# Kernel optimization log

Hardware: AMD Instinct MI355X
Metric: run time of the kernel (lower is better)

## Reference

```python
import jax, jax.numpy as jnp
import numpy as np

N, E, D, L, H = 10000, 160000, 128, 3, 8
DH = D // H
EPS = 1e-5


def ln(x, g, b):
    m = x.mean(-1, keepdims=True)
    v = ((x - m) ** 2).mean(-1, keepdims=True)
    return (x - m) * jax.lax.rsqrt(v + EPS) * g + b


def setup_inputs() -> dict:
    key = jax.random.key(0)
    ks = iter(jax.random.split(key, 16))
    rn = lambda s, sc=0.05: jax.random.normal(next(ks), s, dtype=jnp.float32) * sc
    return {
        'lane_feats': jax.random.normal(next(ks), (N, 10), dtype=jnp.float32),
        'edge_attrs': jax.random.normal(next(ks), (E, 9), dtype=jnp.float32),
        'edge_index': jax.random.randint(next(ks), (2, E), 0, N),
        'node_W': rn((10, D)), 'node_b': jnp.zeros((D,)), 'node_g': jnp.ones((D,)), 'node_bt': jnp.zeros((D,)),
        'rpe_W': rn((9, D)), 'rpe_b': jnp.zeros((D,)), 'rpe_g': jnp.ones((D,)), 'rpe_bt': jnp.zeros((D,)),
        'mem_W': rn((L, 3 * D, D)), 'mem_b': jnp.zeros((L, D)), 'mem_g': jnp.ones((L, D)), 'mem_bt': jnp.zeros((L, D)),
        'Wq': rn((L, D, D)), 'Wk': rn((L, D, D)), 'Wv': rn((L, D, D)), 'Wo': rn((L, D, D)),
        'eu_W': rn((L, D, D)), 'eu_b': jnp.zeros((L, D)), 'eu_g': jnp.ones((L, D)), 'eu_bt': jnp.zeros((L, D)),
        'en_g': jnp.ones((L, D)), 'en_bt': jnp.zeros((L, D)),
        'ffn_W1': rn((L, D, 2 * D)), 'ffn_b1': jnp.zeros((L, 2 * D)),
        'ffn_W2': rn((L, 2 * D, D)), 'ffn_b2': jnp.zeros((L, D)),
        'n1_g': jnp.ones((L, D)), 'n1_bt': jnp.zeros((L, D)),
        'n2_g': jnp.ones((L, D)), 'n2_bt': jnp.zeros((L, D)),
    }


def reference(lane_feats, edge_attrs, edge_index,
              node_W, node_b, node_g, node_bt,
              rpe_W, rpe_b, rpe_g, rpe_bt,
              mem_W, mem_b, mem_g, mem_bt,
              Wq, Wk, Wv, Wo,
              eu_W, eu_b, eu_g, eu_bt,
              en_g, en_bt,
              ffn_W1, ffn_b1, ffn_W2, ffn_b2,
              n1_g, n1_bt, n2_g, n2_bt):
    src, dst = edge_index[0], edge_index[1]
    # input projections (dropout is identity in eval)
    x = jax.nn.relu(ln(lane_feats @ node_W + node_b, node_g, node_bt))  # [N, D]
    e = jax.nn.relu(ln(edge_attrs @ rpe_W + rpe_b, rpe_g, rpe_bt))      # [E, D]
    for l in range(L):
        x_i, x_j = x[dst], x[src]  # receiver / sender features [E, D]
        mem = jax.nn.relu(ln(jnp.concatenate([x_i, x_j, e], axis=-1) @ mem_W[l] + mem_b[l],
                             mem_g[l], mem_bt[l]))
        delta = jax.nn.relu(ln(mem @ eu_W[l] + eu_b[l], eu_g[l], eu_bt[l]))
        e = ln(e + delta, en_g[l], en_bt[l])
        q = (x_i @ Wq[l]).reshape(E, H, DH)
        k = (mem @ Wk[l]).reshape(E, H, DH)
        v = (mem @ Wv[l]).reshape(E, H, DH)
        logits = (q * k).sum(-1) / np.float32(np.sqrt(DH))  # [E, H]
        # segment softmax over destination nodes (pyg_softmax)
        mx = jax.ops.segment_max(logits, dst, num_segments=N)
        ex = jnp.exp(logits - mx[dst])
        sm = jax.ops.segment_sum(ex, dst, num_segments=N)
        attn = ex / (sm[dst] + 1e-16)
        out_e = (attn[..., None] * v).reshape(E, D) @ Wo[l]
        agg = jax.ops.segment_sum(out_e, dst, num_segments=N)  # scatter-add aggregation
        x = ln(x + agg, n1_g[l], n1_bt[l])
        h = jax.nn.relu(x @ ffn_W1[l] + ffn_b1[l]) @ ffn_W2[l] + ffn_b2[l]
        x = ln(x + h, n2_g[l], n2_bt[l])
    return x
```

## Files before the change

### kernel.cpp

```cpp
#include <hip/hip_runtime.h>
#include <cstdint>

#define NN 10000
#define NE 160000
#define DD 128
#define NL 3

typedef __attribute__((ext_vector_type(8))) __bf16 bf16x8;
typedef __attribute__((ext_vector_type(4))) float f32x4;

__device__ __forceinline__ ushort f2bf(float f) {
  unsigned u = __float_as_uint(f);
  return (ushort)((u + 0x7fffu + ((u >> 16) & 1u)) >> 16);
}
__device__ __forceinline__ float bf2f(ushort s) {
  return __uint_as_float(((unsigned)s) << 16);
}
__device__ __forceinline__ float wsum32(float v) {
  v += __shfl_xor(v, 1); v += __shfl_xor(v, 2); v += __shfl_xor(v, 4);
  v += __shfl_xor(v, 8); v += __shfl_xor(v, 16);
  return v;
}
__device__ __forceinline__ float wsum64(float v) {
  v = wsum32(v); v += __shfl_xor(v, 32); return v;
}
__device__ __forceinline__ void red16_2(float& a, float& b) {
#pragma unroll
  for (int m = 1; m < 16; m <<= 1) { a += __shfl_xor(a, m); b += __shfl_xor(b, m); }
}
__device__ __forceinline__ uint4 ldg16(const ushort* p) { return *(const uint4*)p; }

#define PH(id, MAXID, AT, ASTR, KK, AS) {                                       \
    if ((id) < (MAXID)) {                                                       \
      ushort* _db = Bb[((id) + 1) & 1];                                         \
      if ((id) & 1) { *(uint4*)(_db + tid * 8) = sa0;                           \
                      *(uint4*)(_db + 2048 + tid * 8) = sa1; }                  \
      else          { *(uint4*)(_db + tid * 8) = sb0;                           \
                      *(uint4*)(_db + 2048 + tid * 8) = sb1; }                  \
    }                                                                           \
    if ((id) + 2 <= (MAXID)) {                                                  \
      if ((id) & 1) { sb0 = ldg16(csrc((id) + 2, tid));                         \
                      sb1 = ldg16(csrc((id) + 2, 256 + tid)); }                 \
      else          { sa0 = ldg16(csrc((id) + 2, tid));                         \
                      sa1 = ldg16(csrc((id) + 2, 256 + tid)); }                 \
    }                                                                           \
    { bf16x8 _a = *(const bf16x8*)((AT) + (r0 + c) * (ASTR) + (KK) * 32 + g * 8); \
      const ushort* _bp = Bb[(id) & 1] + lane * 8;                              \
      __builtin_amdgcn_s_setprio(1);                                            \
      _Pragma("unroll") for (int _t = 0; _t < 8; ++_t)                          \
        AS[_t] = __builtin_amdgcn_mfma_f32_16x16x32_bf16(                       \
            _a, *(const bf16x8*)(_bp + _t * 512), AS[_t], 0, 0, 0);             \
      __builtin_amdgcn_s_setprio(0); }                                          \
    __syncthreads(); }

__global__ __launch_bounds__(256) void k_hist(const int* __restrict__ dst,
                                              int* __restrict__ deg) {
  int e = blockIdx.x * 256 + threadIdx.x;
  if (e < NE) atomicAdd(&deg[dst[e]], 1);
}

__global__ __launch_bounds__(256) void k_scan(const int* __restrict__ deg,
                                              int* __restrict__ rowptr,
                                              int* __restrict__ cursor) {
  __shared__ int part[256];
  const int t = threadIdx.x;
  const int CH = 40;
  int base = t * CH;
  int s = 0;
  for (int i = 0; i < CH; ++i) {
    int idx = base + i;
    s += (idx < NN) ? deg[idx] : 0;
  }
  part[t] = s;
  __syncthreads();
  for (int off = 1; off < 256; off <<= 1) {
    int v = (t >= off) ? part[t - off] : 0;
    __syncthreads();
    part[t] += v;
    __syncthreads();
  }
  int run = (t == 0) ? 0 : part[t - 1];
  for (int i = 0; i < CH; ++i) {
    int idx = base + i;
    if (idx < NN) {
      rowptr[idx] = run;
      cursor[idx] = run;
      run += deg[idx];
    }
  }
  if (t == 255) rowptr[NN] = part[255];
}

__global__ __launch_bounds__(256) void k_scatter(const int* __restrict__ dst,
                                                 int* __restrict__ cursor,
                                                 int* __restrict__ eids) {
  int e = blockIdx.x * 256 + threadIdx.x;
  if (e < NE) {
    int pos = atomicAdd(&cursor[dst[e]], 1);
    eids[pos] = e;
  }
}

__global__ __launch_bounds__(256) void k_permidx(const int* __restrict__ ei,
                                                 const int* __restrict__ perm,
                                                 int* __restrict__ srcP,
                                                 int* __restrict__ dstP) {
  int i = blockIdx.x * 256 + threadIdx.x;
  if (i < NE) {
    int e = perm[i];
    srcP[i] = ei[e];
    dstP[i] = ei[NE + e];
  }
}

__global__ __launch_bounds__(256) void k_transp(const float* __restrict__ in,
                                                ushort* __restrict__ out,
                                                int K, int N) {
  __shared__ float T[32][33];
  int k0 = blockIdx.x * 32, n0 = blockIdx.y * 32;
  in += (size_t)blockIdx.z * K * N;
  out += (size_t)blockIdx.z * K * N;
  int tx = threadIdx.x & 31, ty = threadIdx.x >> 5;
#pragma unroll
  for (int r = 0; r < 32; r += 8)
    if (k0 + ty + r < K && n0 + tx < N)
      T[ty + r][tx] = in[(size_t)(k0 + ty + r) * N + n0 + tx];
  __syncthreads();
#pragma unroll
  for (int r = 0; r < 32; r += 8)
    if (n0 + ty + r < N && k0 + tx < K)
      out[(size_t)(n0 + ty + r) * K + k0 + tx] = f2bf(T[tx][ty + r]);
}

__global__ __launch_bounds__(256) void k_transp5(
    const float* __restrict__ Wa, const float* __restrict__ Wb,
    const float* __restrict__ Wc, const float* __restrict__ Wd,
    const float* __restrict__ We, ushort* __restrict__ Oa,
    ushort* __restrict__ Ob, ushort* __restrict__ Oc, ushort* __restrict__ Od,
    ushort* __restrict__ Oe) {
  __shared__ float T[32][33];
  int l = blockIdx.z / 5, wsel = blockIdx.z % 5;
  const float* in =
      (wsel == 0 ? Wa : wsel == 1 ? Wb : wsel == 2 ? Wc : wsel == 3 ? Wd : We) +
      (size_t)l * 128 * 128;
  ushort* out =
      (wsel == 0 ? Oa : wsel == 1 ? Ob : wsel == 2 ? Oc : wsel == 3 ? Od : Oe) +
      (size_t)l * 128 * 128;
  int k0 = blockIdx.x * 32, n0 = blockIdx.y * 32;
  int tx = threadIdx.x & 31, ty = threadIdx.x >> 5;
#pragma unroll
  for (int r = 0; r < 32; r += 8)
    T[ty + r][tx] = in[(size_t)(k0 + ty + r) * 128 + n0 + tx];
  __syncthreads();
#pragma unroll
  for (int r = 0; r < 32; r += 8)
    out[(size_t)(n0 + ty + r) * 128 + k0 + tx] = f2bf(T[tx][ty + r]);
}

template <int K>
__global__ __launch_bounds__(256) void k_inproj(
    const float* __restrict__ inp, const int* __restrict__ perm,
    const float* __restrict__ W, const float* __restrict__ b,
    const float* __restrict__ g, const float* __restrict__ bt,
    float* __restrict__ outF, ushort* __restrict__ outB, int rows) {
  int row = blockIdx.x * 4 + (threadIdx.x >> 6);
  if (row >= rows) return;
  int srow = perm ? perm[row] : row;
  int lane = threadIdx.x & 63;
  float a0 = b[lane], a1 = b[lane + 64];
#pragma unroll
  for (int k = 0; k < K; ++k) {
    float xv = inp[(size_t)srow * K + k];
    a0 = fmaf(xv, W[k * DD + lane], a0);
    a1 = fmaf(xv, W[k * DD + lane + 64], a1);
  }
  float m = wsum64(a0 + a1) * (1.0f / DD);
  float q = wsum64(a0 * a0 + a1 * a1) * (1.0f / DD);
  float rstd = rsqrtf(q - m * m + 1e-5f);
  float o0 = fmaxf((a0 - m) * rstd * g[lane] + bt[lane], 0.0f);
  float o1 = fmaxf((a1 - m) * rstd * g[lane + 64] + bt[lane + 64], 0.0f);
  size_t base = (size_t)row * DD;
  if (outF) { outF[base + lane] = o0; outF[base + lane + 64] = o1; }
  outB[base + lane] = f2bf(o0);
  outB[base + lane + 64] = f2bf(o1);
}

__global__ __launch_bounds__(256) void k_nodepre(
    const ushort* __restrict__ xb, const ushort* __restrict__ memWT,
    const ushort* __restrict__ WqT, const float* __restrict__ memB,
    float* __restrict__ Pa, float* __restrict__ Pb, ushort* __restrict__ qbo) {
  __shared__ __align__(16) ushort Xt[64 * 136];
  __shared__ __align__(16) ushort Bb[4096];
  const int tid = threadIdx.x;
  const int n0 = blockIdx.x * 64;
  const int z = blockIdx.y;
  const ushort* B0 = (z == 0) ? memWT : ((z == 1) ? memWT + 128 : WqT);
  const int bstr = (z < 2) ? 384 : 128;
  uint4 w[2], wn[2];
#pragma unroll
  for (int i = 0; i < 2; ++i) {
    int u = tid + i * 256;
    w[i] = ldg16(B0 + (size_t)(u >> 2) * bstr + (u & 3) * 8);
  }
#pragma unroll
  for (int it = 0; it < 4; ++it) {
    int ch = it * 256 + tid, row = ch >> 4, j = ch & 15;
    int gr = n0 + row; if (gr > NN - 1) gr = NN - 1;
    *(uint4*)(Xt + row * 136 + j * 8) = *(const uint4*)(xb + (size_t)gr * DD + j * 8);
  }
  const int lane = tid & 63, wv = tid >> 6;
  const int c = lane & 15, g = lane >> 4, r0 = wv * 16;
  f32x4 acc[8];
#pragma unroll
  for (int t = 0; t < 8; ++t) acc[t] = (f32x4){0.f, 0.f, 0.f, 0.f};
#pragma unroll
  for (int kk = 0; kk < 4; ++kk) {
    __syncthreads();
#pragma unroll
    for (int i = 0; i < 2; ++i) *(uint4*)(Bb + (tid + i * 256) * 8) = w[i];
    if (kk < 3) {
#pragma unroll
      for (int i = 0; i < 2; ++i) {
        int u = tid + i * 256;
        wn[i] = ldg16(B0 + (size_t)(u >> 2) * bstr + (kk + 1) * 32 + (u & 3) * 8);
      }
    }
    __syncthreads();
    bf16x8 a = *(const bf16x8*)(Xt + (r0 + c) * 136 + kk * 32 + g * 8);
#pragma unroll
    for (int t = 0; t < 8; ++t)
      acc[t] = __builtin_amdgcn_mfma_f32_16x16x32_bf16(
          a, *(const bf16x8*)(Bb + (t * 16 + c) * 32 + g * 8), acc[t], 0, 0, 0);
#pragma unroll
    for (int i = 0; i < 2; ++i) w[i] = wn[i];
  }
  if (z == 0) {
#pragma unroll
    for (int t = 0; t < 8; ++t) {
      float bv = memB[t * 16 + c];
#pragma unroll
      for (int rr = 0; rr < 4; ++rr) {
        int row = n0 + r0 + g * 4 + rr;
        if (row < NN) Pa[(size_t)row * DD + t * 16 + c] = acc[t][rr] + bv;
      }
    }
  } else if (z == 1) {
#pragma unroll
    for (int t = 0; t < 8; ++t)
#pragma unroll
      for (int rr = 0; rr < 4; ++rr) {
        int row = n0 + r0 + g * 4 + rr;
        if (row < NN) Pb[(size_t)row * DD + t * 16 + c] = acc[t][rr];
      }
  } else {
#pragma unroll
    for (int t = 0; t < 8; ++t)
#pragma unroll
      for (int rr = 0; rr < 4; ++rr) {
        int row = n0 + r0 + g * 4 + rr;
        if (row < NN) qbo[(size_t)row * DD + t * 16 + c] = f2bf(acc[t][rr]);
      }
  }
}

__global__ __launch_bounds__(256, 3) void k_edge(
    ushort* __restrict__ ebg, ushort* __restrict__ vbg,
    const float* __restrict__ Pa, const float* __restrict__ Pb,
    const ushort* __restrict__ qb, const int* __restrict__ srcP,
    const int* __restrict__ dstP, const ushort* __restrict__ memWT,
    const float* __restrict__ memG, const float* __restrict__ memBt,
    const ushort* __restrict__ euWT, const float* __restrict__ euB,
    const float* __restrict__ euG, const float* __restrict__ euBt,
    const float* __restrict__ enG, const float* __restrict__ enBt,
    const ushort* __restrict__ WkT, const ushort* __restrict__ WvT,
    float* __restrict__ lg) {
  __shared__ __align__(16) ushort Et[64 * 136];
  __shared__ __align__(16) ushort Mt[64 * 136];
  __shared__ __align__(16) ushort Bb[2][4096];
  const int tid = threadIdx.x;
  const int e0 = blockIdx.x * 64;
  const int lane = tid & 63, wv = tid >> 6;
  const int c = lane & 15, g = lane >> 4, r0 = wv * 16;

  auto csrc = [&](int j, int u) -> const ushort* {
    const ushort* base; int stride, off, kk = j & 3;
    if (j < 4)       { base = memWT; stride = 384; off = 256 + kk * 32; }
    else if (j < 8)  { base = euWT;  stride = 128; off = kk * 32; }
    else if (j < 12) { base = WkT;   stride = 128; off = kk * 32; }
    else             { base = WvT;   stride = 128; off = kk * 32; }
    return base + ((u >> 6) * 16 + (u & 15)) * stride + off + ((u >> 4) & 3) * 8;
  };

  int dv[4], sv[4];
#pragma unroll
  for (int rr = 0; rr < 4; ++rr) {
    int row = e0 + r0 + g * 4 + rr;
    dv[rr] = dstP[row]; sv[rr] = srcP[row];
  }
  uint4 sa0 = ldg16(csrc(0, tid)), sa1 = ldg16(csrc(0, 256 + tid));
  uint4 sb0 = ldg16(csrc(1, tid)), sb1 = ldg16(csrc(1, 256 + tid));
#pragma unroll
  for (int it = 0; it < 4; ++it) {
    int ch = it * 256 + tid, row = ch >> 4, j = ch & 15;
    *(uint4*)(Et + row * 136 + j * 8) =
        *(const uint4*)(ebg + (size_t)(e0 + row) * DD + j * 8);
  }
  *(uint4*)(Bb[0] + tid * 8) = sa0;
  *(uint4*)(Bb[0] + 2048 + tid * 8) = sa1;
  __syncthreads();

  f32x4 acc[8];

#pragma unroll
  for (int t = 0; t < 8; ++t) acc[t] = (f32x4){0.f, 0.f, 0.f, 0.f};
  PH(0, 15, Et, 136, 0, acc)
  PH(1, 15, Et, 136, 1, acc)
  PH(2, 15, Et, 136, 2, acc)
  PH(3, 15, Et, 136, 3, acc)

  {
    float ps[8][4];
#pragma unroll
    for (int t = 0; t < 8; ++t)
#pragma unroll
      for (int rr = 0; rr < 4; ++rr)
        ps[t][rr] = Pa[(size_t)dv[rr] * DD + t * 16 + c] +
                    Pb[(size_t)sv[rr] * DD + t * 16 + c];
    float s1[4] = {0, 0, 0, 0}, s2[4] = {0, 0, 0, 0};
#pragma unroll
    for (int t = 0; t < 8; ++t)
#pragma unroll
      for (int rr = 0; rr < 4; ++rr) {
        float s = acc[t][rr] + ps[t][rr];
        acc[t][rr] = s; s1[rr] += s; s2[rr] += s * s;
      }
    float mean[4], rstd[4];
#pragma unroll
    for (int rr = 0; rr < 4; ++rr) {
      red16_2(s1[rr], s2[rr]);
      mean[rr] = s1[rr] * (1.f / DD);
      rstd[rr] = rsqrtf(s2[rr] * (1.f / DD) - mean[rr] * mean[rr] + 1e-5f);
    }
#pragma unroll
    for (int t = 0; t < 8; ++t) {
      float gv = memG[t * 16 + c], tv = memBt[t * 16 + c];
#pragma unroll
      for (int rr = 0; rr < 4; ++rr) {
        float o = fmaxf((acc[t][rr] - mean[rr]) * rstd[rr] * gv + tv, 0.f);
        Mt[(r0 + g * 4 + rr) * 136 + t * 16 + c] = f2bf(o);
      }
    }
  }
  __syncthreads();

#pragma unroll
  for (int t = 0; t < 8; ++t) acc[t] = (f32x4){0.f, 0.f, 0.f, 0.f};
  PH(4, 15, Mt, 136, 0, acc)
  PH(5, 15, Mt, 136, 1, acc)
  PH(6, 15, Mt, 136, 2, acc)
  PH(7, 15, Mt, 136, 3, acc)

  {
    float s1[4] = {0, 0, 0, 0}, s2[4] = {0, 0, 0, 0};
#pragma unroll
    for (int t = 0; t < 8; ++t) {
      float bv = euB[t * 16 + c];
#pragma unroll
      for (int rr = 0; rr < 4; ++rr) {
        float v2 = acc[t][rr] + bv;
        acc[t][rr] = v2; s1[rr] += v2; s2[rr] += v2 * v2;
      }
    }
    float mean[4], rstd[4];
#pragma unroll
    for (int rr = 0; rr < 4; ++rr) {
      red16_2(s1[rr], s2[rr]);
      mean[rr] = s1[rr] * (1.f / DD);
      rstd[rr] = rsqrtf(s2[rr] * (1.f / DD) - mean[rr] * mean[rr] + 1e-5f);
    }
    float t1[4] = {0, 0, 0, 0}, t2[4] = {0, 0, 0, 0};
#pragma unroll
    for (int t = 0; t < 8; ++t) {
      float gv = euG[t * 16 + c], tv = euBt[t * 16 + c];
#pragma unroll
      for (int rr = 0; rr < 4; ++rr) {
        float d = fmaxf((acc[t][rr] - mean[rr]) * rstd[rr] * gv + tv, 0.f);
        float eo = bf2f(Et[(r0 + g * 4 + rr) * 136 + t * 16 + c]);
        float pv = eo + d;
        acc[t][rr] = pv; t1[rr] += pv; t2[rr] += pv * pv;
      }
    }
    float mean3[4], rstd3[4];
#pragma unroll
    for (int rr = 0; rr < 4; ++rr) {
      red16_2(t1[rr], t2[rr]);
      mean3[rr] = t1[rr] * (1.f / DD);
      rstd3[rr] = rsqrtf(t2[rr] * (1.f / DD) - mean3[rr] * mean3[rr] + 1e-5f);
    }
#pragma unroll
    for (int t = 0; t < 8; ++t) {
      float gv = enG[t * 16 + c], tv = enBt[t * 16 + c];
#pragma unroll
      for (int rr = 0; rr < 4; ++rr) {
        float en = (acc[t][rr] - mean3[rr]) * rstd3[rr] * gv + tv;
        Et[(r0 + g * 4 + rr) * 136 + t * 16 + c] = f2bf(en);
      }
    }
  }
  __syncthreads();
#pragma unroll
  for (int it = 0; it < 4; ++it) {
    int ch = it * 256 + tid, row = ch >> 4, j = ch & 15;
    *(uint4*)(ebg + (size_t)(e0 + row) * DD + j * 8) =
        *(const uint4*)(Et + row * 136 + j * 8);
  }

  float qvf[8][4];
#pragma unroll
  for (int t = 0; t < 8; ++t)
#pragma unroll
    for (int rr = 0; rr < 4; ++rr)
      qvf[t][rr] = bf2f(qb[(size_t)dv[rr] * DD + t * 16 + c]);

#pragma unroll
  for (int t = 0; t < 8; ++t) acc[t] = (f32x4){0.f, 0.f, 0.f, 0.f};
  PH(8, 15, Mt, 136, 0, acc)
  PH(9, 15, Mt, 136, 1, acc)
  PH(10, 15, Mt, 136, 2, acc)
  PH(11, 15, Mt, 136, 3, acc)
#pragma unroll
  for (int t = 0; t < 8; ++t) {
    float p[4];
#pragma unroll
    for (int rr = 0; rr < 4; ++rr) p[rr] = acc[t][rr] * qvf[t][rr];
#pragma unroll
    for (int m = 1; m < 16; m <<= 1)
#pragma unroll
      for (int rr = 0; rr < 4; ++rr) p[rr] += __shfl_xor(p[rr], m);
    if (c == t) {
#pragma unroll
      for (int rr = 0; rr < 4; ++rr)
        lg[(size_t)(e0 + r0 + g * 4 + rr) * 8 + t] = p[rr] * 0.25f;
    }
  }

#pragma unroll
  for (int t = 0; t < 8; ++t) acc[t] = (f32x4){0.f, 0.f, 0.f, 0.f};
  PH(12, 15, Mt, 136, 0, acc)
  PH(13, 15, Mt, 136, 1, acc)
  PH(14, 15, Mt, 136, 2, acc)
  PH(15, 15, Mt, 136, 3, acc)
#pragma unroll
  for (int t = 0; t < 8; ++t)
#pragma unroll
    for (int rr = 0; rr < 4; ++rr)
      Et[(r0 + g * 4 + rr) * 136 + t * 16 + c] = f2bf(acc[t][rr]);
  __syncthreads();
#pragma unroll
  for (int it = 0; it < 4; ++it) {
    int ch = it * 256 + tid, row = ch >> 4, j = ch & 15;
    *(uint4*)(vbg + (size_t)(e0 + row) * DD + j * 8) =
        *(const uint4*)(Et + row * 136 + j * 8);
  }
}

__global__ __launch_bounds__(256) void k_aggr(
    const ushort* __restrict__ vbg, float* __restrict__ lg,
    const int* __restrict__ rowptr, float* __restrict__ agg) {
  int node = blockIdx.x * 4 + (threadIdx.x >> 6);
  if (node >= NN) return;
  const int lane = threadIdx.x & 63;
  const int j = lane & 7, h = lane >> 3;
  const int beg = rowptr[node], end = rowptr[node + 1];
  float mx = -3.4e38f;
  for (int i = beg + j; i < end; i += 8)
    mx = fmaxf(mx, lg[(size_t)i * 8 + h]);
  mx = fmaxf(mx, __shfl_xor(mx, 1));
  mx = fmaxf(mx, __shfl_xor(mx, 2));
  mx = fmaxf(mx, __shfl_xor(mx, 4));
  float sm = 0.f;
  for (int i = beg + j; i < end; i += 8) {
    float ex = expf(lg[(size_t)i * 8 + h] - mx);
    lg[(size_t)i * 8 + h] = ex;
    sm += ex;
  }
  sm += __shfl_xor(sm, 1);
  sm += __shfl_xor(sm, 2);
  sm += __shfl_xor(sm, 4);
  float inv = 1.f / (sm + 1e-16f);
  asm volatile("s_waitcnt vmcnt(0)" ::: "memory");
  float acc0 = 0.f, acc1 = 0.f;
  for (int i = beg; i < end; ++i) {
    float w = lg[(size_t)i * 8 + h] * inv;
    ushort2 vv = *(const ushort2*)(vbg + (size_t)i * DD + lane * 2);
    acc0 = fmaf(bf2f(vv.x), w, acc0);
    acc1 = fmaf(bf2f(vv.y), w, acc1);
  }
  *(float2*)(agg + (size_t)node * DD + lane * 2) = make_float2(acc0, acc1);
}

__global__ __launch_bounds__(256) void k_node2(
    const float* __restrict__ vagg, const ushort* __restrict__ WoT,
    const float* __restrict__ xres_g, const float* __restrict__ g1,
    const float* __restrict__ bt1, const ushort* __restrict__ W1T,
    const float* __restrict__ b1, const ushort* __restrict__ W2T,
    const float* __restrict__ b2, const float* __restrict__ g2,
    const float* __restrict__ bt2, float* __restrict__ out,
    ushort* __restrict__ outB) {
  __shared__ __align__(16) ushort Xt[64 * 136];
  __shared__ __align__(16) ushort Hs[64 * 264];
  __shared__ __align__(16) ushort Bb[8192];
  const int tid = threadIdx.x;
  const int n0 = blockIdx.x * 64;
  const int lane = tid & 63, wv = tid >> 6;
  const int c = lane & 15, g = lane >> 4, r0 = wv * 16;

  float xres[8][4];
#pragma unroll
  for (int t = 0; t < 8; ++t)
#pragma unroll
    for (int rr = 0; rr < 4; ++rr) {
      int row = n0 + r0 + g * 4 + rr;
      if (row > NN - 1) row = NN - 1;
      xres[t][rr] = xres_g[(size_t)row * DD + t * 16 + c];
    }
  uint4 w[4], wn[4];
#pragma unroll
  for (int i = 0; i < 2; ++i) {
    int u = tid + i * 256;
    w[i] = ldg16(WoT + (size_t)(u >> 2) * 128 + (u & 3) * 8);
  }
#pragma unroll
  for (int it = 0; it < 8; ++it) {
    int ch = it * 256 + tid, row = ch >> 5, j = ch & 31;
    int gr = n0 + row; if (gr > NN - 1) gr = NN - 1;
    float4 vv = *(const float4*)(vagg + (size_t)gr * DD + j * 4);
    ushort4 ov; ov.x = f2bf(vv.x); ov.y = f2bf(vv.y); ov.z = f2bf(vv.z); ov.w = f2bf(vv.w);
    *(ushort4*)(Xt + row * 136 + j * 4) = ov;
  }
  f32x4 acc0[8];
#pragma unroll
  for (int t = 0; t < 8; ++t) acc0[t] = (f32x4){0.f, 0.f, 0.f, 0.f};
#pragma unroll
  for (int kk = 0; kk < 4; ++kk) {
    __syncthreads();
#pragma unroll
    for (int i = 0; i < 2; ++i) *(uint4*)(Bb + (tid + i * 256) * 8) = w[i];
    if (kk < 3) {
#pragma unroll
      for (int i = 0; i < 2; ++i) {
        int u = tid + i * 256;
        wn[i] = ldg16(WoT + (size_t)(u >> 2) * 128 + (kk + 1) * 32 + (u & 3) * 8);
      }
    }
    __syncthreads();
    bf16x8 a = *(const bf16x8*)(Xt + (r0 + c) * 136 + kk * 32 + g * 8);
#pragma unroll
    for (int t = 0; t < 8; ++t)
      acc0[t] = __builtin_amdgcn_mfma_f32_16x16x32_bf16(
          a, *(const bf16x8*)(Bb + (t * 16 + c) * 32 + g * 8), acc0[t], 0, 0, 0);
#pragma unroll
    for (int i = 0; i < 2; ++i) w[i] = wn[i];
  }
  {
    float s1[4] = {0, 0, 0, 0}, s2[4] = {0, 0, 0, 0};
#pragma unroll
    for (int t = 0; t < 8; ++t)
#pragma unroll
      for (int rr = 0; rr < 4; ++rr) {
        float s = acc0[t][rr] + xres[t][rr];
        acc0[t][rr] = s; s1[rr] += s; s2[rr] += s * s;
      }
    float mean[4], rstd[4];
#pragma unroll
    for (int rr = 0; rr < 4; ++rr) {
      red16_2(s1[rr], s2[rr]);
      mean[rr] = s1[rr] * (1.f / DD);
      rstd[rr] = rsqrtf(s2[rr] * (1.f / DD) - mean[rr] * mean[rr] + 1e-5f);
    }
#pragma unroll
    for (int t = 0; t < 8; ++t) {
      float gv = g1[t * 16 + c], tv = bt1[t * 16 + c];
#pragma unroll
      for (int rr = 0; rr < 4; ++rr) {
        float o = (acc0[t][rr] - mean[rr]) * rstd[rr] * gv + tv;
        Xt[(r0 + g * 4 + rr) * 136 + t * 16 + c] = f2bf(o);
      }
    }
  }
  f32x4 acc16[16];
#pragma unroll
  for (int t = 0; t < 16; ++t) acc16[t] = (f32x4){0.f, 0.f, 0.f, 0.f};
#pragma unroll
  for (int i = 0; i < 4; ++i) {
    int u = tid + i * 256;
    w[i] = ldg16(W1T + (size_t)(u >> 2) * 128 + (u & 3) * 8);
  }
#pragma unroll
  for (int kk = 0; kk < 4; ++kk) {
    __syncthreads();
#pragma unroll
    for (int i = 0; i < 4; ++i) *(uint4*)(Bb + (tid + i * 256) * 8) = w[i];
    if (kk < 3) {
#pragma unroll
      for (int i = 0; i < 4; ++i) {
        int u = tid + i * 256;
        wn[i] = ldg16(W1T + (size_t)(u >> 2) * 128 + (kk + 1) * 32 + (u & 3) * 8);
      }
    }
    __syncthreads();
    bf16x8 a = *(const bf16x8*)(Xt + (r0 + c) * 136 + kk * 32 + g * 8);
#pragma unroll
    for (int t = 0; t < 16; ++t)
      acc16[t] = __builtin_amdgcn_mfma_f32_16x16x32_bf16(
          a, *(const bf16x8*)(Bb + (t * 16 + c) * 32 + g * 8), acc16[t], 0, 0, 0);
#pragma unroll
    for (int i = 0; i < 4; ++i) w[i] = wn[i];
  }
#pragma unroll
  for (int t = 0; t < 16; ++t) {
    float bv = b1[t * 16 + c];
#pragma unroll
    for (int rr = 0; rr < 4; ++rr)
      Hs[(r0 + g * 4 + rr) * 264 + t * 16 + c] = f2bf(fmaxf(acc16[t][rr] + bv, 0.f));
  }
#pragma unroll
  for (int t = 0; t < 8; ++t) acc0[t] = (f32x4){0.f, 0.f, 0.f, 0.f};
#pragma unroll
  for (int i = 0; i < 2; ++i) {
    int u = tid + i * 256;
    w[i] = ldg16(W2T + (size_t)(u >> 2) * 256 + (u & 3) * 8);
  }
#pragma unroll
  for (int kk = 0; kk < 8; ++kk) {
    __syncthreads();
#pragma unroll
    for (int i = 0; i < 2; ++i) *(uint4*)(Bb + (tid + i * 256) * 8) = w[i];
    if (kk < 7) {
#pragma unroll
      for (int i = 0; i < 2; ++i) {
        int u = tid + i * 256;
        wn[i] = ldg16(W2T + (size_t)(u >> 2) * 256 + (kk + 1) * 32 + (u & 3) * 8);
      }
    }
    __syncthreads();
    bf16x8 a = *(const bf16x8*)(Hs + (r0 + c) * 264 + kk * 32 + g * 8);
#pragma unroll
    for (int t = 0; t < 8; ++t)
      acc0[t] = __builtin_amdgcn_mfma_f32_16x16x32_bf16(
          a, *(const bf16x8*)(Bb + (t * 16 + c) * 32 + g * 8), acc0[t], 0, 0, 0);
#pragma unroll
    for (int i = 0; i < 2; ++i) w[i] = wn[i];
  }
  {
    float s1[4] = {0, 0, 0, 0}, s2[4] = {0, 0, 0, 0};
#pragma unroll
    for (int t = 0; t < 8; ++t) {
      float bv = b2[t * 16 + c];
#pragma unroll
      for (int rr = 0; rr < 4; ++rr) {
        float s = acc0[t][rr] + bv + bf2f(Xt[(r0 + g * 4 + rr) * 136 + t * 16 + c]);
        acc0[t][rr] = s; s1[rr] += s; s2[rr] += s * s;
      }
    }
    float mean[4], rstd[4];
#pragma unroll
    for (int rr = 0; rr < 4; ++rr) {
      red16_2(s1[rr], s2[rr]);
      mean[rr] = s1[rr] * (1.f / DD);
      rstd[rr] = rsqrtf(s2[rr] * (1.f / DD) - mean[rr] * mean[rr] + 1e-5f);
    }
#pragma unroll
    for (int t = 0; t < 8; ++t) {
      float gv = g2[t * 16 + c], tv = bt2[t * 16 + c];
#pragma unroll
      for (int rr = 0; rr < 4; ++rr) {
        float o = (acc0[t][rr] - mean[rr]) * rstd[rr] * gv + tv;
        int row = n0 + r0 + g * 4 + rr;
        if (row < NN) out[(size_t)row * DD + t * 16 + c] = o;
        Xt[(r0 + g * 4 + rr) * 136 + t * 16 + c] = f2bf(o);
      }
    }
  }
  __syncthreads();
#pragma unroll
  for (int it = 0; it < 4; ++it) {
    int ch = it * 256 + tid, row = ch >> 4, j = ch & 15;
    int gr = n0 + row;
    if (gr < NN)
      *(uint4*)(outB + (size_t)gr * DD + j * 8) = *(const uint4*)(Xt + row * 136 + j * 8);
  }
}

extern "C" void kernel_launch(void* const* d_in, const int* in_sizes, int n_in,
                              void* d_out, int out_size, void* d_ws,
                              size_t ws_size, hipStream_t stream) {
  (void)in_sizes; (void)n_in; (void)out_size; (void)ws_size;
  const float* lane_feats = (const float*)d_in[0];
  const float* edge_attrs = (const float*)d_in[1];
  const int* ei = (const int*)d_in[2];
  const int* dst = ei + NE;
  const float* node_W = (const float*)d_in[3];
  const float* node_b = (const float*)d_in[4];
  const float* node_g = (const float*)d_in[5];
  const float* node_bt = (const float*)d_in[6];
  const float* rpe_W = (const float*)d_in[7];
  const float* rpe_b = (const float*)d_in[8];
  const float* rpe_g = (const float*)d_in[9];
  const float* rpe_bt = (const float*)d_in[10];
  const float* mem_W = (const float*)d_in[11];
  const float* mem_b = (const float*)d_in[12];
  const float* mem_g = (const float*)d_in[13];
  const float* mem_bt = (const float*)d_in[14];
  const float* Wq = (const float*)d_in[15];
  const float* Wk = (const float*)d_in[16];
  const float* Wv = (const float*)d_in[17];
  const float* Wo = (const float*)d_in[18];
  const float* eu_W = (const float*)d_in[19];
  const float* eu_b = (const float*)d_in[20];
  const float* eu_g = (const float*)d_in[21];
  const float* eu_bt = (const float*)d_in[22];
  const float* en_g = (const float*)d_in[23];
  const float* en_bt = (const float*)d_in[24];
  const float* ffn_W1 = (const float*)d_in[25];
  const float* ffn_b1 = (const float*)d_in[26];
  const float* ffn_W2 = (const float*)d_in[27];
  const float* ffn_b2 = (const float*)d_in[28];
  const float* n1_g = (const float*)d_in[29];
  const float* n1_bt = (const float*)d_in[30];
  const float* n2_g = (const float*)d_in[31];
  const float* n2_bt = (const float*)d_in[32];

  char* p = (char*)d_ws;
  auto alloc = [&](size_t bytes) -> char* {
    char* r = p; p += (bytes + 255) & ~(size_t)255; return r;
  };
  float* x = (float*)alloc((size_t)NN * DD * 4);
  float* vagg = (float*)alloc((size_t)NN * DD * 4);
  float* lg = (float*)alloc((size_t)NE * 8 * 4);
  float* Pa = (float*)alloc((size_t)NN * DD * 4);
  float* Pb = (float*)alloc((size_t)NN * DD * 4);
  ushort* qb = (ushort*)alloc((size_t)NN * DD * 2);
  ushort* xb = (ushort*)alloc((size_t)NN * DD * 2);
  ushort* eb = (ushort*)alloc((size_t)NE * DD * 2);
  ushort* vb = (ushort*)alloc((size_t)NE * DD * 2);
  ushort* memWT = (ushort*)alloc((size_t)NL * DD * 384 * 2);
  ushort* euWT = (ushort*)alloc((size_t)NL * DD * DD * 2);
  ushort* WqT = (ushort*)alloc((size_t)NL * DD * DD * 2);
  ushort* WkT = (ushort*)alloc((size_t)NL * DD * DD * 2);
  ushort* WvT = (ushort*)alloc((size_t)NL * DD * DD * 2);
  ushort* WoT = (ushort*)alloc((size_t)NL * DD * DD * 2);
  ushort* W1T = (ushort*)alloc((size_t)NL * 256 * DD * 2);
  ushort* W2T = (ushort*)alloc((size_t)NL * DD * 256 * 2);
  int* deg = (int*)alloc((size_t)NN * 4);
  int* rowptr = (int*)alloc((size_t)(NN + 1) * 4);
  int* cursor = (int*)alloc((size_t)NN * 4);
  int* eids = (int*)alloc((size_t)NE * 4);
  int* srcP = (int*)alloc((size_t)NE * 4);
  int* dstP = (int*)alloc((size_t)NE * 4);

  hipMemsetAsync(deg, 0, (size_t)NN * 4, stream);
  k_hist<<<NE / 256, 256, 0, stream>>>(dst, deg);
  k_scan<<<1, 256, 0, stream>>>(deg, rowptr, cursor);
  k_scatter<<<NE / 256, 256, 0, stream>>>(dst, cursor, eids);
  k_permidx<<<NE / 256, 256, 0, stream>>>(ei, eids, srcP, dstP);

  k_transp<<<dim3(12, 4, NL), 256, 0, stream>>>(mem_W, memWT, 384, DD);
  k_transp5<<<dim3(4, 4, 5 * NL), 256, 0, stream>>>(
      Wq, Wk, Wv, Wo, eu_W, WqT, WkT, WvT, WoT, euWT);
  k_transp<<<dim3(4, 8, NL), 256, 0, stream>>>(ffn_W1, W1T, DD, 256);
  k_transp<<<dim3(8, 4, NL), 256, 0, stream>>>(ffn_W2, W2T, 256, DD);

  k_inproj<10><<<NN / 4, 256, 0, stream>>>(lane_feats, nullptr, node_W, node_b,
                                           node_g, node_bt, x, xb, NN);
  k_inproj<9><<<NE / 4, 256, 0, stream>>>(edge_attrs, eids, rpe_W, rpe_b,
                                          rpe_g, rpe_bt, nullptr, eb, NE);

  const int NB = (NN + 63) / 64;
  for (int l = 0; l < NL; ++l) {
    k_nodepre<<<dim3(NB, 3), 256, 0, stream>>>(
        xb, memWT + (size_t)l * DD * 384, WqT + (size_t)l * DD * DD,
        mem_b + l * DD, Pa, Pb, qb);
    k_edge<<<NE / 64, 256, 0, stream>>>(
        eb, vb, Pa, Pb, qb, srcP, dstP, memWT + (size_t)l * DD * 384,
        mem_g + l * DD, mem_bt + l * DD, euWT + (size_t)l * DD * DD,
        eu_b + l * DD, eu_g + l * DD, eu_bt + l * DD, en_g + l * DD,
        en_bt + l * DD, WkT + (size_t)l * DD * DD, WvT + (size_t)l * DD * DD,
        lg);
    k_aggr<<<(NN + 3) / 4, 256, 0, stream>>>(vb, lg, rowptr, vagg);
    k_node2<<<NB, 256, 0, stream>>>(
        vagg, WoT + (size_t)l * DD * DD, x, n1_g + l * DD, n1_bt + l * DD,
        W1T + (size_t)l * 256 * DD, ffn_b1 + l * 256,
        W2T + (size_t)l * DD * 256, ffn_b2 + l * DD, n2_g + l * DD,
        n2_bt + l * DD, (l == NL - 1) ? (float*)d_out : x, xb);
  }
}
```

Measured before the change: 509.2 us.

## Shrink edge kernel to 32-edge tiles with single-buffered weight staging

The edge kernel now runs 128-thread blocks covering 32 edges each, twice as many blocks, and drops the double-buffered shared weight tile in favour of one buffer fenced by two barriers per phase. Each thread prefetches the next weight slice into registers while the current slice is consumed. The smaller shared footprint and block size are meant to raise occupancy and spread the edge work across more blocks. In exchange each weight slice is read from global/L2 by twice as many blocks, and the extra barriers per phase can expose load latency.

```diff
diff --git a/kernel.cpp b/kernel.cpp
--- a/kernel.cpp
+++ b/kernel.cpp
@@ -30,28 +30,26 @@
 }
 __device__ __forceinline__ uint4 ldg16(const ushort* p) { return *(const uint4*)p; }
 
-#define PH(id, MAXID, AT, ASTR, KK, AS) {                                       \
-    if ((id) < (MAXID)) {                                                       \
-      ushort* _db = Bb[((id) + 1) & 1];                                         \
-      if ((id) & 1) { *(uint4*)(_db + tid * 8) = sa0;                           \
-                      *(uint4*)(_db + 2048 + tid * 8) = sa1; }                  \
-      else          { *(uint4*)(_db + tid * 8) = sb0;                           \
-                      *(uint4*)(_db + 2048 + tid * 8) = sb1; }                  \
+#define PH1(id, MAXID, AT, KK, AS) {                                            \
+    __syncthreads();                                                            \
+    *(uint4*)(Bb + tid * 8) = w0;                                               \
+    *(uint4*)(Bb + 1024 + tid * 8) = w1;                                        \
+    *(uint4*)(Bb + 2048 + tid * 8) = w2;                                        \
+    *(uint4*)(Bb + 3072 + tid * 8) = w3;                                        \
+    if ((id) + 1 <= (MAXID)) {                                                  \
+      w0 = ldg16(csrc((id) + 1, tid));                                          \
+      w1 = ldg16(csrc((id) + 1, 128 + tid));                                    \
+      w2 = ldg16(csrc((id) + 1, 256 + tid));                                    \
+      w3 = ldg16(csrc((id) + 1, 384 + tid));                                    \
     }                                                                           \
-    if ((id) + 2 <= (MAXID)) {                                                  \
-      if ((id) & 1) { sb0 = ldg16(csrc((id) + 2, tid));                         \
-                      sb1 = ldg16(csrc((id) + 2, 256 + tid)); }                 \
-      else          { sa0 = ldg16(csrc((id) + 2, tid));                         \
-                      sa1 = ldg16(csrc((id) + 2, 256 + tid)); }                 \
-    }                                                                           \
-    { bf16x8 _a = *(const bf16x8*)((AT) + (r0 + c) * (ASTR) + (KK) * 32 + g * 8); \
-      const ushort* _bp = Bb[(id) & 1] + lane * 8;                              \
+    __syncthreads();                                                            \
+    { bf16x8 _a = *(const bf16x8*)((AT) + (r0 + c) * 136 + (KK) * 32 + g * 8);  \
+      const ushort* _bp = Bb + lane * 8;                                        \
       __builtin_amdgcn_s_setprio(1);                                            \
       _Pragma("unroll") for (int _t = 0; _t < 8; ++_t)                          \
         AS[_t] = __builtin_amdgcn_mfma_f32_16x16x32_bf16(                       \
             _a, *(const bf16x8*)(_bp + _t * 512), AS[_t], 0, 0, 0);             \
-      __builtin_amdgcn_s_setprio(0); }                                          \
-    __syncthreads(); }
+      __builtin_amdgcn_s_setprio(0); } }
 
 __global__ __launch_bounds__(256) void k_hist(const int* __restrict__ dst,
                                               int* __restrict__ deg) {
@@ -263,7 +261,7 @@
   }
 }
 
-__global__ __launch_bounds__(256, 3) void k_edge(
+__global__ __launch_bounds__(128, 3) void k_edge(
     ushort* __restrict__ ebg, ushort* __restrict__ vbg,
     const float* __restrict__ Pa, const float* __restrict__ Pb,
     const ushort* __restrict__ qb, const int* __restrict__ srcP,
@@ -274,11 +272,11 @@
     const float* __restrict__ enG, const float* __restrict__ enBt,
     const ushort* __restrict__ WkT, const ushort* __restrict__ WvT,
     float* __restrict__ lg) {
-  __shared__ __align__(16) ushort Et[64 * 136];
-  __shared__ __align__(16) ushort Mt[64 * 136];
-  __shared__ __align__(16) ushort Bb[2][4096];
+  __shared__ __align__(16) ushort Et[32 * 136];
+  __shared__ __align__(16) ushort Mt[32 * 136];
+  __shared__ __align__(16) ushort Bb[4096];
   const int tid = threadIdx.x;
-  const int e0 = blockIdx.x * 64;
+  const int e0 = blockIdx.x * 32;
   const int lane = tid & 63, wv = tid >> 6;
   const int c = lane & 15, g = lane >> 4, r0 = wv * 16;
 
@@ -297,26 +295,23 @@
     int row = e0 + r0 + g * 4 + rr;
     dv[rr] = dstP[row]; sv[rr] = srcP[row];
   }
-  uint4 sa0 = ldg16(csrc(0, tid)), sa1 = ldg16(csrc(0, 256 + tid));
-  uint4 sb0 = ldg16(csrc(1, tid)), sb1 = ldg16(csrc(1, 256 + tid));
+  uint4 w0 = ldg16(csrc(0, tid)), w1 = ldg16(csrc(0, 128 + tid));
+  uint4 w2 = ldg16(csrc(0, 256 + tid)), w3 = ldg16(csrc(0, 384 + tid));
 #pragma unroll
   for (int it = 0; it < 4; ++it) {
-    int ch = it * 256 + tid, row = ch >> 4, j = ch & 15;
+    int ch = it * 128 + tid, row = ch >> 4, j = ch & 15;
     *(uint4*)(Et + row * 136 + j * 8) =
         *(const uint4*)(ebg + (size_t)(e0 + row) * DD + j * 8);
   }
-  *(uint4*)(Bb[0] + tid * 8) = sa0;
-  *(uint4*)(Bb[0] + 2048 + tid * 8) = sa1;
-  __syncthreads();
 
   f32x4 acc[8];
 
 #pragma unroll
   for (int t = 0; t < 8; ++t) acc[t] = (f32x4){0.f, 0.f, 0.f, 0.f};
-  PH(0, 15, Et, 136, 0, acc)
-  PH(1, 15, Et, 136, 1, acc)
-  PH(2, 15, Et, 136, 2, acc)
-  PH(3, 15, Et, 136, 3, acc)
+  PH1(0, 15, Et, 0, acc)
+  PH1(1, 15, Et, 1, acc)
+  PH1(2, 15, Et, 2, acc)
+  PH1(3, 15, Et, 3, acc)
 
   {
     float ps[8][4];
@@ -351,14 +346,13 @@
       }
     }
   }
-  __syncthreads();
 
 #pragma unroll
   for (int t = 0; t < 8; ++t) acc[t] = (f32x4){0.f, 0.f, 0.f, 0.f};
-  PH(4, 15, Mt, 136, 0, acc)
-  PH(5, 15, Mt, 136, 1, acc)
-  PH(6, 15, Mt, 136, 2, acc)
-  PH(7, 15, Mt, 136, 3, acc)
+  PH1(4, 15, Mt, 0, acc)
+  PH1(5, 15, Mt, 1, acc)
+  PH1(6, 15, Mt, 2, acc)
+  PH1(7, 15, Mt, 3, acc)
 
   {
     float s1[4] = {0, 0, 0, 0}, s2[4] = {0, 0, 0, 0};
@@ -410,7 +404,7 @@
   __syncthreads();
 #pragma unroll
   for (int it = 0; it < 4; ++it) {
-    int ch = it * 256 + tid, row = ch >> 4, j = ch & 15;
+    int ch = it * 128 + tid, row = ch >> 4, j = ch & 15;
     *(uint4*)(ebg + (size_t)(e0 + row) * DD + j * 8) =
         *(const uint4*)(Et + row * 136 + j * 8);
   }
@@ -424,10 +418,10 @@
 
 #pragma unroll
   for (int t = 0; t < 8; ++t) acc[t] = (f32x4){0.f, 0.f, 0.f, 0.f};
-  PH(8, 15, Mt, 136, 0, acc)
-  PH(9, 15, Mt, 136, 1, acc)
-  PH(10, 15, Mt, 136, 2, acc)
-  PH(11, 15, Mt, 136, 3, acc)
+  PH1(8, 15, Mt, 0, acc)
+  PH1(9, 15, Mt, 1, acc)
+  PH1(10, 15, Mt, 2, acc)
+  PH1(11, 15, Mt, 3, acc)
 #pragma unroll
   for (int t = 0; t < 8; ++t) {
     float p[4];
@@ -446,10 +440,10 @@
 
 #pragma unroll
   for (int t = 0; t < 8; ++t) acc[t] = (f32x4){0.f, 0.f, 0.f, 0.f};
-  PH(12, 15, Mt, 136, 0, acc)
-  PH(13, 15, Mt, 136, 1, acc)
-  PH(14, 15, Mt, 136, 2, acc)
-  PH(15, 15, Mt, 136, 3, acc)
+  PH1(12, 15, Mt, 0, acc)
+  PH1(13, 15, Mt, 1, acc)
+  PH1(14, 15, Mt, 2, acc)
+  PH1(15, 15, Mt, 3, acc)
 #pragma unroll
   for (int t = 0; t < 8; ++t)
 #pragma unroll
@@ -458,7 +452,7 @@
   __syncthreads();
 #pragma unroll
   for (int it = 0; it < 4; ++it) {
-    int ch = it * 256 + tid, row = ch >> 4, j = ch & 15;
+    int ch = it * 128 + tid, row = ch >> 4, j = ch & 15;
     *(uint4*)(vbg + (size_t)(e0 + row) * DD + j * 8) =
         *(const uint4*)(Et + row * 136 + j * 8);
   }
@@ -781,7 +775,7 @@
     k_nodepre<<<dim3(NB, 3), 256, 0, stream>>>(
         xb, memWT + (size_t)l * DD * 384, WqT + (size_t)l * DD * DD,
         mem_b + l * DD, Pa, Pb, qb);
-    k_edge<<<NE / 64, 256, 0, stream>>>(
+    k_edge<<<NE / 32, 128, 0, stream>>>(
         eb, vb, Pa, Pb, qb, srcP, dstP, memWT + (size_t)l * DD * 384,
         mem_g + l * DD, mem_bt + l * DD, euWT + (size_t)l * DD * DD,
         eu_b + l * DD, eu_g + l * DD, eu_bt + l * DD, en_g + l * DD,
```

Measured after the change: 708.7 us. 1.39x slower.
